# Optimization experiments

Measured on AMD Instinct MI355X. Metric: run time of the kernel, lower is better.

The kernel has to match this reference:

```python
import jax, jax.numpy as jnp
import numpy as np

B, N, D = 256, 196, 768  # batch, num_patches (14x14 grid), patch_dim (16*16*3)


def setup_inputs() -> dict:
    key = jax.random.key(0)
    k1, k2 = jax.random.split(key)
    features = jax.random.normal(k1, (B, N, D), dtype=jnp.float32)
    position_logits = jax.random.normal(k2, (B, N, N), dtype=jnp.float32)
    return {"features": features, "position_logits": position_logits}


def _rearrange_patches(patches, pos):
    # Deterministic gather form: for each target slot p, take the LARGEST j with
    # pos[i, j] == p, else leave the zero-init.
    b, n, d = patches.shape
    j_ids = jnp.arange(n, dtype=jnp.int32)
    match = pos[:, :, None] == jnp.arange(n)[None, None, :]          # [B, j, p]
    winner = jnp.max(jnp.where(match, j_ids[None, :, None], -1), axis=1)  # [B, p]
    gathered = jnp.take_along_axis(patches, jnp.clip(winner, 0)[:, :, None], axis=1)
    return jnp.where(winner[:, :, None] >= 0, gathered, jnp.zeros((), patches.dtype))


def reference(features, position_logits):
    b, n, d = features.shape
    g = int(n ** 0.5)
    # _get_position_predictions: argmax / max-softmax over dim=1 (position classes)
    pos = jnp.argmax(position_logits, axis=1)                         # [B, N] int
    confidence = jnp.max(jax.nn.softmax(position_logits, axis=1), axis=1)  # [B, N]
    # _rearrange_patches (scatter by predicted position)
    patches = _rearrange_patches(features, pos)
    # _smooth_edges: 3-tap average over interior patch indices, reading originals
    mid = (patches[:, :-2] + patches[:, 1:-1] + patches[:, 2:]) / 3.0
    patches = jnp.concatenate([patches[:, :1], mid, patches[:, -1:]], axis=1)
    # _reconstruct_image: [B, g, g, D] -> [B, D, g, g]
    img = patches.reshape(b, g, g, d).transpose(0, 3, 1, 2)
    return img, confidence
```

## Files before the change

kernel.cpp:

```cpp
#include <hip/hip_runtime.h>
#include <math.h>

#define BB 256
#define NN 196
#define DD 768
#define TDK 32
#define NHALF 2
#define DHALF (DD / NHALF)
#define NTILES (DHALF / TDK)
#define SROW 224
#define NW 8
#define NITEMS (NN * 8)

typedef float f32x4 __attribute__((ext_vector_type(4)));

__global__ __launch_bounds__(512) void fused_kernel(
    const float* __restrict__ features,
    const float* __restrict__ logits,
    float* __restrict__ img,
    float* __restrict__ conf_out)
{
    const int b = blockIdx.x;
    const int h = blockIdx.y;
    const int t = threadIdx.x;

    __shared__ float sm[NW][NN];
    __shared__ float ss[NW][NN];
    __shared__ int   si[NW][NN];
    __shared__ int   winner_s[NN];
    __shared__ float tile[TDK * SROW];

    const int wv = t >> 6;
    const int l  = t & 63;

    if (t < NN) winner_s[t] = -1;

    {
        const int i0 = (49 * wv) >> 1;
        const int i1 = (49 * (wv + 1)) >> 1;
        if (l < 49) {
            const float* basep = logits + (size_t)b * NN * NN + 4 * l;
            f32x4 m = {-INFINITY, -INFINITY, -INFINITY, -INFINITY};
            f32x4 s = {0.f, 0.f, 0.f, 0.f};
            int4 idx = make_int4(0, 0, 0, 0);
            #pragma unroll 4
            for (int i = i0; i < i1; ++i) {
                const f32x4 x = *reinterpret_cast<const f32x4*>(basep + (size_t)i * NN);
                f32x4 mn;
                mn.x = fmaxf(m.x, x.x); mn.y = fmaxf(m.y, x.y);
                mn.z = fmaxf(m.z, x.z); mn.w = fmaxf(m.w, x.w);
                idx.x = (x.x > m.x) ? i : idx.x;
                idx.y = (x.y > m.y) ? i : idx.y;
                idx.z = (x.z > m.z) ? i : idx.z;
                idx.w = (x.w > m.w) ? i : idx.w;
                s.x = s.x * __expf(m.x - mn.x) + __expf(x.x - mn.x);
                s.y = s.y * __expf(m.y - mn.y) + __expf(x.y - mn.y);
                s.z = s.z * __expf(m.z - mn.z) + __expf(x.z - mn.z);
                s.w = s.w * __expf(m.w - mn.w) + __expf(x.w - mn.w);
                m = mn;
            }
            const int c = 4 * l;
            sm[wv][c + 0] = m.x; ss[wv][c + 0] = s.x; si[wv][c + 0] = idx.x;
            sm[wv][c + 1] = m.y; ss[wv][c + 1] = s.y; si[wv][c + 1] = idx.y;
            sm[wv][c + 2] = m.z; ss[wv][c + 2] = s.z; si[wv][c + 2] = idx.z;
            sm[wv][c + 3] = m.w; ss[wv][c + 3] = s.w; si[wv][c + 3] = idx.w;
        }
    }
    __syncthreads();

    if (t < NN) {
        const int j = t;
        float m = -INFINITY;
        int idx = 0;
        #pragma unroll
        for (int ww = 0; ww < NW; ++ww) {
            const float mg = sm[ww][j];
            if (mg > m) { m = mg; idx = si[ww][j]; }
        }
        float s = 0.0f;
        #pragma unroll
        for (int ww = 0; ww < NW; ++ww)
            s += ss[ww][j] * __expf(sm[ww][j] - m);
        if (h == 0) conf_out[b * NN + j] = 1.0f / s;
        atomicMax(&winner_s[idx], j);
    }
    __syncthreads();

    const float* fb = features + (size_t)b * NN * DD;
    const int D0 = h * DHALF;
    float* ob = img + (size_t)b * DD * NN + (size_t)D0 * NN;

    int  rr[4], k4[4], wn[4];
    bool act[4];
    #pragma unroll
    for (int i = 0; i < 4; ++i) {
        const int item = t + 512 * i;
        act[i] = (item < NITEMS);
        rr[i]  = act[i] ? (item >> 3) : 0;
        k4[i]  = (item & 7) * 4;
        wn[i]  = act[i] ? winner_s[rr[i]] : -1;
    }

    const f32x4 zero = {0.f, 0.f, 0.f, 0.f};
    f32x4 cur[4], nxt[4];
    #pragma unroll
    for (int i = 0; i < 4; ++i)
        cur[i] = (wn[i] >= 0)
            ? *reinterpret_cast<const f32x4*>(fb + (size_t)wn[i] * DD + D0 + k4[i])
            : zero;

    for (int kt = 0; kt < NTILES; ++kt) {
        #pragma unroll
        for (int i = 0; i < 4; ++i) {
            if (act[i]) {
                const int r  = rr[i];
                const int kb = k4[i] >> 2;
                const int col = (((r >> 2) ^ kb) << 2) + (r & 3);
                tile[(k4[i] + 0) * SROW + col] = cur[i].x;
                tile[(k4[i] + 1) * SROW + col] = cur[i].y;
                tile[(k4[i] + 2) * SROW + col] = cur[i].z;
                tile[(k4[i] + 3) * SROW + col] = cur[i].w;
            }
        }
        #pragma unroll
        for (int i = 0; i < 4; ++i) nxt[i] = zero;
        if (kt + 1 < NTILES) {
            const int dn = D0 + (kt + 1) * TDK;
            #pragma unroll
            for (int i = 0; i < 4; ++i)
                if (wn[i] >= 0)
                    nxt[i] = *reinterpret_cast<const f32x4*>(fb + (size_t)wn[i] * DD + dn + k4[i]);
        }
        __syncthreads();

        const int dg0 = kt * TDK;
        #pragma unroll
        for (int it = 0; it < 4; ++it) {
            const int q = t + 512 * it;
            if (q < TDK * 49) {
                const int dl  = q / 49;
                const int c   = q - 49 * dl;
                const int key = (dl >> 2) & 7;
                const float* row = &tile[dl * SROW];
                const f32x4 ctr = *reinterpret_cast<const f32x4*>(row + ((c ^ key) << 2));
                const float left  = (c > 0)  ? row[(((c - 1) ^ key) << 2) + 3] : 0.0f;
                const float right = (c < 48) ? row[ ((c + 1) ^ key) << 2      ] : 0.0f;
                const int p0 = 4 * c;
                f32x4 o;
                o.x = (p0 == 0)          ? ctr.x : (left  + ctr.x + ctr.y) * (1.0f / 3.0f);
                o.y = (ctr.x + ctr.y + ctr.z) * (1.0f / 3.0f);
                o.z = (ctr.y + ctr.z + ctr.w) * (1.0f / 3.0f);
                o.w = (p0 + 3 == NN - 1) ? ctr.w : (ctr.z + ctr.w + right) * (1.0f / 3.0f);
                float* dst = ob + (size_t)(dg0 + dl) * NN + p0;
                __builtin_nontemporal_store(o, reinterpret_cast<f32x4*>(dst));
            }
        }
        #pragma unroll
        for (int i = 0; i < 4; ++i) cur[i] = nxt[i];
        __syncthreads();
    }
}

extern "C" void kernel_launch(void* const* d_in, const int* in_sizes, int n_in,
                              void* d_out, int out_size, void* d_ws, size_t ws_size,
                              hipStream_t stream) {
    const float* features = (const float*)d_in[0];
    const float* logits   = (const float*)d_in[1];

    float* out  = (float*)d_out;
    float* img  = out;
    float* conf = out + (size_t)BB * DD * NN;

    dim3 grid(BB, NHALF);
    fused_kernel<<<grid, 512, 0, stream>>>(features, logits, img, conf);
}
```

Measured before the change: 50.92 us.

## Double-buffer LDS tile and use a single LDS-only barrier per iteration

The transpose tile becomes two LDS buffers that alternate per D-tile. This drops the trailing __syncthreads in each loop iteration. The remaining barrier is a custom one that waits only on LDS counters (lgkmcnt), so the prefetch of the next tile's features from global memory can stay in flight across it. The tile buffers share storage, through a union, with the softmax reduction scratch to limit LDS growth, and the swizzled column index is hoisted out of the loop. The risk is subtle ordering bugs if the compiler or barrier semantics differ from what is assumed. The gain may also be small if the kernel is already near bandwidth.

```diff
diff --git a/kernel.cpp b/kernel.cpp
--- a/kernel.cpp
+++ b/kernel.cpp
@@ -9,10 +9,16 @@
 #define DHALF (DD / NHALF)
 #define NTILES (DHALF / TDK)
 #define SROW 224
+#define NITEMS (NN * 8)
 #define NW 8
-#define NITEMS (NN * 8)
 
 typedef float f32x4 __attribute__((ext_vector_type(4)));
+
+__device__ __forceinline__ void lds_barrier() {
+    asm volatile("s_waitcnt lgkmcnt(0)" ::: "memory");
+    __builtin_amdgcn_s_barrier();
+    asm volatile("" ::: "memory");
+}
 
 __global__ __launch_bounds__(512) void fused_kernel(
     const float* __restrict__ features,
@@ -24,11 +30,11 @@
     const int h = blockIdx.y;
     const int t = threadIdx.x;
 
-    __shared__ float sm[NW][NN];
-    __shared__ float ss[NW][NN];
-    __shared__ int   si[NW][NN];
-    __shared__ int   winner_s[NN];
-    __shared__ float tile[TDK * SROW];
+    __shared__ union {
+        struct { float sm[NW][NN]; float ss[NW][NN]; int si[NW][NN]; } a;
+        float tiles[2][TDK * SROW];
+    } u;
+    __shared__ int winner_s[NN];
 
     const int wv = t >> 6;
     const int l  = t & 63;
@@ -60,10 +66,10 @@
                 m = mn;
             }
             const int c = 4 * l;
-            sm[wv][c + 0] = m.x; ss[wv][c + 0] = s.x; si[wv][c + 0] = idx.x;
-            sm[wv][c + 1] = m.y; ss[wv][c + 1] = s.y; si[wv][c + 1] = idx.y;
-            sm[wv][c + 2] = m.z; ss[wv][c + 2] = s.z; si[wv][c + 2] = idx.z;
-            sm[wv][c + 3] = m.w; ss[wv][c + 3] = s.w; si[wv][c + 3] = idx.w;
+            u.a.sm[wv][c + 0] = m.x; u.a.ss[wv][c + 0] = s.x; u.a.si[wv][c + 0] = idx.x;
+            u.a.sm[wv][c + 1] = m.y; u.a.ss[wv][c + 1] = s.y; u.a.si[wv][c + 1] = idx.y;
+            u.a.sm[wv][c + 2] = m.z; u.a.ss[wv][c + 2] = s.z; u.a.si[wv][c + 2] = idx.z;
+            u.a.sm[wv][c + 3] = m.w; u.a.ss[wv][c + 3] = s.w; u.a.si[wv][c + 3] = idx.w;
         }
     }
     __syncthreads();
@@ -74,13 +80,13 @@
         int idx = 0;
         #pragma unroll
         for (int ww = 0; ww < NW; ++ww) {
-            const float mg = sm[ww][j];
-            if (mg > m) { m = mg; idx = si[ww][j]; }
+            const float mg = u.a.sm[ww][j];
+            if (mg > m) { m = mg; idx = u.a.si[ww][j]; }
         }
         float s = 0.0f;
         #pragma unroll
         for (int ww = 0; ww < NW; ++ww)
-            s += ss[ww][j] * __expf(sm[ww][j] - m);
+            s += u.a.ss[ww][j] * __expf(u.a.sm[ww][j] - m);
         if (h == 0) conf_out[b * NN + j] = 1.0f / s;
         atomicMax(&winner_s[idx], j);
     }
@@ -90,7 +96,7 @@
     const int D0 = h * DHALF;
     float* ob = img + (size_t)b * DD * NN + (size_t)D0 * NN;
 
-    int  rr[4], k4[4], wn[4];
+    int  rr[4], k4[4], wn[4], col[4];
     bool act[4];
     #pragma unroll
     for (int i = 0; i < 4; ++i) {
@@ -99,6 +105,7 @@
         rr[i]  = act[i] ? (item >> 3) : 0;
         k4[i]  = (item & 7) * 4;
         wn[i]  = act[i] ? winner_s[rr[i]] : -1;
+        col[i] = (((rr[i] >> 2) ^ (k4[i] >> 2)) << 2) + (rr[i] & 3);
     }
 
     const f32x4 zero = {0.f, 0.f, 0.f, 0.f};
@@ -110,18 +117,18 @@
             : zero;
 
     for (int kt = 0; kt < NTILES; ++kt) {
+        float* buf = u.tiles[kt & 1];
+
         #pragma unroll
         for (int i = 0; i < 4; ++i) {
             if (act[i]) {
-                const int r  = rr[i];
-                const int kb = k4[i] >> 2;
-                const int col = (((r >> 2) ^ kb) << 2) + (r & 3);
-                tile[(k4[i] + 0) * SROW + col] = cur[i].x;
-                tile[(k4[i] + 1) * SROW + col] = cur[i].y;
-                tile[(k4[i] + 2) * SROW + col] = cur[i].z;
-                tile[(k4[i] + 3) * SROW + col] = cur[i].w;
+                buf[(k4[i] + 0) * SROW + col[i]] = cur[i].x;
+                buf[(k4[i] + 1) * SROW + col[i]] = cur[i].y;
+                buf[(k4[i] + 2) * SROW + col[i]] = cur[i].z;
+                buf[(k4[i] + 3) * SROW + col[i]] = cur[i].w;
             }
         }
+
         #pragma unroll
         for (int i = 0; i < 4; ++i) nxt[i] = zero;
         if (kt + 1 < NTILES) {
@@ -131,17 +138,18 @@
                 if (wn[i] >= 0)
                     nxt[i] = *reinterpret_cast<const f32x4*>(fb + (size_t)wn[i] * DD + dn + k4[i]);
         }
-        __syncthreads();
+
+        lds_barrier();
 
         const int dg0 = kt * TDK;
         #pragma unroll
         for (int it = 0; it < 4; ++it) {
             const int q = t + 512 * it;
-            if (q < TDK * 49) {
+            if (q < NITEMS) {
                 const int dl  = q / 49;
                 const int c   = q - 49 * dl;
                 const int key = (dl >> 2) & 7;
-                const float* row = &tile[dl * SROW];
+                const float* row = &buf[dl * SROW];
                 const f32x4 ctr = *reinterpret_cast<const f32x4*>(row + ((c ^ key) << 2));
                 const float left  = (c > 0)  ? row[(((c - 1) ^ key) << 2) + 3] : 0.0f;
                 const float right = (c < 48) ? row[ ((c + 1) ^ key) << 2      ] : 0.0f;
@@ -151,13 +159,11 @@
                 o.y = (ctr.x + ctr.y + ctr.z) * (1.0f / 3.0f);
                 o.z = (ctr.y + ctr.z + ctr.w) * (1.0f / 3.0f);
                 o.w = (p0 + 3 == NN - 1) ? ctr.w : (ctr.z + ctr.w + right) * (1.0f / 3.0f);
-                float* dst = ob + (size_t)(dg0 + dl) * NN + p0;
-                __builtin_nontemporal_store(o, reinterpret_cast<f32x4*>(dst));
+                __builtin_nontemporal_store(o, reinterpret_cast<f32x4*>(ob + (size_t)(dg0 + dl) * NN + p0));
             }
         }
         #pragma unroll
         for (int i = 0; i < 4; ++i) cur[i] = nxt[i];
-        __syncthreads();
     }
 }
 
```

Measured after the change: 50.93 us. Within noise of the previous version (+0.0%).
